# Optimization experiments

Measured on AMD Instinct MI355X. Metric: run time of the kernel, lower is better.

The kernel has to match this reference:

```python
import jax, jax.numpy as jnp
import numpy as np

N_AP, N_UE, D = 256, 1024, 64  # dimension = 64 in source

def setup_inputs() -> dict:
    key = jax.random.key(0)
    ks = jax.random.split(key, 9)
    s = 1.0 / np.sqrt(2 * D)
    return {
        "ap_hid": jax.random.normal(ks[0], (N_AP, D), jnp.float32),
        "ue_hid": jax.random.normal(ks[1], (N_UE, D), jnp.float32),
        "edge_hid": jax.random.normal(ks[2], (N_AP, N_UE, D), jnp.float32),
        "W1": jax.random.normal(ks[3], (2 * D, D), jnp.float32) * s,
        "b1": jnp.zeros((D,), jnp.float32),
        "W2": jax.random.normal(ks[4], (2 * D, D), jnp.float32) * s,
        "b2": jnp.zeros((D,), jnp.float32),
        "W3": jax.random.normal(ks[5], (2 * D, D), jnp.float32) * s,
        "b3": jnp.zeros((D,), jnp.float32),
    }

def reference(ap_hid, ue_hid, edge_hid, W1, b1, W2, b2, W3, b3):
    # edge_hid[a, u] is the feature of edge (AP a, UE u); eid is (a, u) itself.
    A, U, d = edge_hid.shape

    # reduce_func_ap: per-AP mailbox over all UE neighbors -> mlp1(cat(ap_hid, edge_hid))
    ap_in = jnp.concatenate(
        [jnp.broadcast_to(ap_hid[:, None, :], (A, U, d)), edge_hid], axis=-1)  # [A,U,2d]
    ap_res = jax.nn.relu(jnp.einsum('auk,kd->aud', ap_in, W1) + b1)            # [A,U,d]

    # reduce_func_ue: per-UE mailbox over all AP neighbors -> mlp2(cat(ue_hid, edge_hid))
    edge_ua = jnp.swapaxes(edge_hid, 0, 1)                                     # [U,A,d]
    ue_in = jnp.concatenate(
        [jnp.broadcast_to(ue_hid[:, None, :], (U, A, d)), edge_ua], axis=-1)   # [U,A,2d]
    ue_res = jax.nn.relu(jnp.einsum('uak,kd->uad', ue_in, W2) + b2)            # [U,A,d]

    # message_func_edge: for edge (a,u), sum src AP's ap_result excluding the
    # mailbox slot whose eid matches this edge, plus same for dst UE's ue_result.
    ap_sum = ap_res.sum(axis=1)   # [A,d]
    ue_sum = ue_res.sum(axis=1)   # [U,d]
    agg = (ap_sum[:, None, :] - ap_res) \
        + (ue_sum[None, :, :] - jnp.swapaxes(ue_res, 0, 1))                     # [A,U,d]

    new = jnp.einsum('auk,kd->aud', jnp.concatenate([edge_hid, agg], axis=-1), W3) + b3
    return new  # new edge 'hid' for both AP2UE and UE2AP, shape [A,U,d]
```

## Files before the change

### kernel.cpp

```cpp
#include <hip/hip_runtime.h>


#define A_N 256
#define U_N 1024

typedef short short8 __attribute__((ext_vector_type(8)));
typedef float f32x4 __attribute__((ext_vector_type(4)));

__device__ __forceinline__ unsigned short f2bf(float f) {
  unsigned int u = __float_as_uint(f);
  return (unsigned short)((u + 0x7FFFu + ((u >> 16) & 1u)) >> 16);
}

__device__ __forceinline__ f32x4 mfma16(short8 a, short8 b, f32x4 c) {
  return __builtin_amdgcn_mfma_f32_16x16x32_bf16(a, b, c, 0, 0, 0);
}

__device__ __forceinline__ void cvt16(const float4& e0, const float4& e1,
                                      const float4& e2, const float4& e3,
                                      short8& a0, short8& a1) {
  a0[0] = (short)f2bf(e0.x); a0[1] = (short)f2bf(e0.y);
  a0[2] = (short)f2bf(e0.z); a0[3] = (short)f2bf(e0.w);
  a0[4] = (short)f2bf(e1.x); a0[5] = (short)f2bf(e1.y);
  a0[6] = (short)f2bf(e1.z); a0[7] = (short)f2bf(e1.w);
  a1[0] = (short)f2bf(e2.x); a1[1] = (short)f2bf(e2.y);
  a1[2] = (short)f2bf(e2.z); a1[3] = (short)f2bf(e2.w);
  a1[4] = (short)f2bf(e3.x); a1[5] = (short)f2bf(e3.y);
  a1[6] = (short)f2bf(e3.z); a1[7] = (short)f2bf(e3.w);
}

__device__ __forceinline__ void rowmlp_row(const float* __restrict__ in,
                                           const float* __restrict__ W,
                                           const float* __restrict__ bias,
                                           float* __restrict__ out, int r, int lane) {
  float rv = in[r * 64 + lane];
  float acc = bias ? bias[lane] : 0.f;
#pragma unroll
  for (int k = 0; k < 64; k++) acc += __shfl(rv, k, 64) * W[k * 64 + lane];
  out[r * 64 + lane] = acc;
}

__global__ __launch_bounds__(256) void k_prep(
    const float* __restrict__ ap_hid, const float* __restrict__ ue_hid,
    const float* __restrict__ W1, const float* __restrict__ b1,
    const float* __restrict__ W2, const float* __restrict__ b2,
    const float* __restrict__ W3, unsigned short* __restrict__ Wt,
    float* __restrict__ acc_zero, float* __restrict__ c1, float* __restrict__ c2) {
  int bx = blockIdx.x, tid = threadIdx.x;
  if (bx < 320) {
    int i = bx * 256 + tid;
    if (i < 81920) acc_zero[i] = 0.f;
  } else if (bx < 384) {
    int idx = (bx - 320) * 256 + tid;
    int r = idx >> 6, k = idx & 63;
    int sec = r >> 6, d = r & 63;
    float v;
    if (sec == 0)      v = W1[(64 + k) * 64 + d];
    else if (sec == 1) v = W2[(64 + k) * 64 + d];
    else if (sec == 2) v = W3[k * 64 + d];
    else               v = W3[(64 + k) * 64 + d];
    Wt[r * 64 + k] = f2bf(v);
  } else if (bx < 448) {
    int r = (bx - 384) * 4 + (tid >> 6);
    rowmlp_row(ap_hid, W1, b1, c1, r, tid & 63);
  } else {
    int r = (bx - 448) * 4 + (tid >> 6);
    rowmlp_row(ue_hid, W2, b2, c2, r, tid & 63);
  }
}

__global__ __launch_bounds__(256) void k_post(
    const float* __restrict__ ap_sum, const float* __restrict__ ue_sum,
    const float* __restrict__ W3, const float* __restrict__ b3,
    float* __restrict__ s3, float* __restrict__ s4) {
  int bx = blockIdx.x, tid = threadIdx.x;
  if (bx < 64) {
    int r = bx * 4 + (tid >> 6);
    rowmlp_row(ap_sum, W3 + 4096, nullptr, s3, r, tid & 63);
  } else {
    int r = (bx - 64) * 4 + (tid >> 6);
    rowmlp_row(ue_sum, W3 + 4096, b3, s4, r, tid & 63);
  }
}

__global__ __launch_bounds__(256) void k_pass1(
    const float* __restrict__ edge, const unsigned short* __restrict__ Wt,
    const float* __restrict__ c1, const float* __restrict__ c2,
    float* __restrict__ ap_sum, float* __restrict__ ue_sum) {
  int tid = threadIdx.x, lane = tid & 63, w = tid >> 6;
  int fr = lane & 15, fq = lane >> 4;
  int a0 = (blockIdx.x >> 4) * 4;
  int u0 = (blockIdx.x & 15) * 64;
  int urow = u0 + w * 16 + fr;
  const float* erow = edge + urow * 64 + fq * 8;

  short8 bw[8][2];
#pragma unroll
  for (int nt = 0; nt < 8; nt++)
#pragma unroll
    for (int ks = 0; ks < 2; ks++)
      bw[nt][ks] = *(const short8*)(Wt + (nt * 16 + fr) * 64 + ks * 32 + fq * 8);

  float c2v[4][4];
#pragma unroll
  for (int j = 0; j < 4; j++)
#pragma unroll
    for (int i = 0; i < 4; i++)
      c2v[j][i] = c2[(u0 + w * 16 + fq * 4 + i) * 64 + j * 16 + fr];

  float ureg[4][4];
#pragma unroll
  for (int j = 0; j < 4; j++)
#pragma unroll
    for (int i = 0; i < 4; i++) ureg[j][i] = 0.f;

  const float* p0 = erow + a0 * 65536;
  float4 e0 = *(const float4*)(p0);
  float4 e1 = *(const float4*)(p0 + 4);
  float4 e2 = *(const float4*)(p0 + 32);
  float4 e3 = *(const float4*)(p0 + 36);
  float c1v[4];
#pragma unroll
  for (int j = 0; j < 4; j++) c1v[j] = c1[a0 * 64 + j * 16 + fr];

  for (int c = 0; c < 4; c++) {
    int a = a0 + c;
    float4 n0, n1, n2, n3;
    float nc1[4];
    if (c < 3) {
      const float* np = erow + (a + 1) * 65536;
      n0 = *(const float4*)(np);
      n1 = *(const float4*)(np + 4);
      n2 = *(const float4*)(np + 32);
      n3 = *(const float4*)(np + 36);
#pragma unroll
      for (int j = 0; j < 4; j++) nc1[j] = c1[(a + 1) * 64 + j * 16 + fr];
    }
    short8 af0, af1;
    cvt16(e0, e1, e2, e3, af0, af1);

#pragma unroll
    for (int j = 0; j < 4; j++) {
      f32x4 acc = {0.f, 0.f, 0.f, 0.f};
      acc = mfma16(af0, bw[j][0], acc);
      acc = mfma16(af1, bw[j][1], acc);
      float cv = c1v[j];
      float rs = fmaxf(acc[0] + cv, 0.f) + fmaxf(acc[1] + cv, 0.f) +
                 fmaxf(acc[2] + cv, 0.f) + fmaxf(acc[3] + cv, 0.f);
      rs += __shfl_xor(rs, 16, 64);
      rs += __shfl_xor(rs, 32, 64);
      if (lane < 16) atomicAdd(&ap_sum[a * 64 + j * 16 + lane], rs);
    }
#pragma unroll
    for (int j = 0; j < 4; j++) {
      f32x4 acc = {0.f, 0.f, 0.f, 0.f};
      acc = mfma16(af0, bw[4 + j][0], acc);
      acc = mfma16(af1, bw[4 + j][1], acc);
#pragma unroll
      for (int i = 0; i < 4; i++)
        ureg[j][i] += fmaxf(acc[i] + c2v[j][i], 0.f);
    }
    if (c < 3) {
      e0 = n0; e1 = n1; e2 = n2; e3 = n3;
#pragma unroll
      for (int j = 0; j < 4; j++) c1v[j] = nc1[j];
    }
  }
#pragma unroll
  for (int j = 0; j < 4; j++)
#pragma unroll
    for (int i = 0; i < 4; i++)
      atomicAdd(&ue_sum[(u0 + w * 16 + fq * 4 + i) * 64 + j * 16 + fr], ureg[j][i]);
}

__global__ __launch_bounds__(256) void k_pass2(
    const float* __restrict__ edge, const unsigned short* __restrict__ Wt,
    const float* __restrict__ c1, const float* __restrict__ c2,
    const float* __restrict__ s3, const float* __restrict__ s4,
    float* __restrict__ out) {
  __shared__ unsigned short W_lds[256 * 72];
  __shared__ unsigned short t_lds[64 * 72];
  int tid = threadIdx.x, lane = tid & 63, w = tid >> 6;
  int fr = lane & 15, fq = lane >> 4;
  int a = blockIdx.x >> 2;
  int ubase = (blockIdx.x & 3) * 256;

#pragma unroll
  for (int it = 0; it < 8; it++) {
    int r = it * 32 + (tid >> 3), seg = tid & 7;
    *(uint4*)&W_lds[r * 72 + seg * 8] = *(const uint4*)(Wt + r * 64 + seg * 8);
  }

  float c1v[4], s3v[4];
#pragma unroll
  for (int j = 0; j < 4; j++) {
    c1v[j] = c1[a * 64 + j * 16 + fr];
    s3v[j] = s3[a * 64 + j * 16 + fr];
  }

  const float* er0 = edge + (a * 1024 + ubase + w * 16 + fr) * 64 + fq * 8;
  float4 e0 = *(const float4*)(er0);
  float4 e1 = *(const float4*)(er0 + 4);
  float4 e2 = *(const float4*)(er0 + 32);
  float4 e3 = *(const float4*)(er0 + 36);

  __syncthreads();

  for (int pnl = 0; pnl < 4; pnl++) {
    int upan = ubase + pnl * 64;
    float4 n0, n1, n2, n3;
    if (pnl < 3) {
      const float* nr = edge + (a * 1024 + upan + 64 + w * 16 + fr) * 64 + fq * 8;
      n0 = *(const float4*)(nr);
      n1 = *(const float4*)(nr + 4);
      n2 = *(const float4*)(nr + 32);
      n3 = *(const float4*)(nr + 36);
    }
    float c2v[4][4], s4v[4][4];
#pragma unroll
    for (int j = 0; j < 4; j++)
#pragma unroll
      for (int i = 0; i < 4; i++) {
        int u = upan + w * 16 + fq * 4 + i;
        c2v[j][i] = c2[u * 64 + j * 16 + fr];
        s4v[j][i] = s4[u * 64 + j * 16 + fr];
      }
    short8 af0, af1;
    cvt16(e0, e1, e2, e3, af0, af1);

    f32x4 accP3[4];
#pragma unroll
    for (int j = 0; j < 4; j++) {
      const unsigned short* wr = &W_lds[(j * 16 + fr) * 72 + fq * 8];
      short8 b10 = *(const short8*)(wr);
      short8 b11 = *(const short8*)(wr + 32);
      short8 b20 = *(const short8*)(wr + 64 * 72);
      short8 b21 = *(const short8*)(wr + 64 * 72 + 32);
      short8 b30 = *(const short8*)(wr + 128 * 72);
      short8 b31 = *(const short8*)(wr + 128 * 72 + 32);
      f32x4 a1 = {0.f, 0.f, 0.f, 0.f};
      a1 = mfma16(af0, b10, a1);
      a1 = mfma16(af1, b11, a1);
      f32x4 a2 = {0.f, 0.f, 0.f, 0.f};
      a2 = mfma16(af0, b20, a2);
      a2 = mfma16(af1, b21, a2);
      f32x4 p3 = {0.f, 0.f, 0.f, 0.f};
      p3 = mfma16(af0, b30, p3);
      p3 = mfma16(af1, b31, p3);
      accP3[j] = p3;
#pragma unroll
      for (int i = 0; i < 4; i++) {
        float tv = fmaxf(a1[i] + c1v[j], 0.f) + fmaxf(a2[i] + c2v[j][i], 0.f);
        t_lds[(w * 16 + fq * 4 + i) * 72 + j * 16 + fr] = f2bf(tv);
      }
    }
    short8 tf0 = *(const short8*)&t_lds[(w * 16 + fr) * 72 + fq * 8];
    short8 tf1 = *(const short8*)&t_lds[(w * 16 + fr) * 72 + 32 + fq * 8];
#pragma unroll
    for (int j = 0; j < 4; j++) {
      const unsigned short* wr = &W_lds[(192 + j * 16 + fr) * 72 + fq * 8];
      short8 b0 = *(const short8*)(wr);
      short8 b1 = *(const short8*)(wr + 32);
      f32x4 acc = {0.f, 0.f, 0.f, 0.f};
      acc = mfma16(tf0, b0, acc);
      acc = mfma16(tf1, b1, acc);
#pragma unroll
      for (int i = 0; i < 4; i++) {
        int u = upan + w * 16 + fq * 4 + i;
        out[(a * 1024 + u) * 64 + j * 16 + fr] =
            accP3[j][i] - acc[i] + s3v[j] + s4v[j][i];
      }
    }
    if (pnl < 3) { e0 = n0; e1 = n1; e2 = n2; e3 = n3; }
  }
}

extern "C" void kernel_launch(void* const* d_in, const int* in_sizes, int n_in,
                              void* d_out, int out_size, void* d_ws, size_t ws_size,
                              hipStream_t stream) {
  const float* ap_hid = (const float*)d_in[0];
  const float* ue_hid = (const float*)d_in[1];
  const float* edge   = (const float*)d_in[2];
  const float* W1     = (const float*)d_in[3];
  const float* b1     = (const float*)d_in[4];
  const float* W2     = (const float*)d_in[5];
  const float* b2     = (const float*)d_in[6];
  const float* W3     = (const float*)d_in[7];
  const float* b3     = (const float*)d_in[8];
  float* out = (float*)d_out;

  char* ws = (char*)d_ws;
  unsigned short* Wt = (unsigned short*)ws;
  float* c1     = (float*)(ws + 32768);
  float* c2     = (float*)(ws + 98304);
  float* ap_sum = (float*)(ws + 360448);
  float* ue_sum = (float*)(ws + 425984);
  float* s3     = (float*)(ws + 688128);
  float* s4     = (float*)(ws + 753664);

  k_prep<<<704, 256, 0, stream>>>(ap_hid, ue_hid, W1, b1, W2, b2, W3, Wt,
                                  (float*)(ws + 360448), c1, c2);
  k_pass1<<<1024, 256, 0, stream>>>(edge, Wt, c1, c2, ap_sum, ue_sum);
  k_post<<<320, 256, 0, stream>>>(ap_sum, ue_sum, W3, b3, s3, s4);
  k_pass2<<<1024, 256, 0, stream>>>(edge, Wt, c1, c2, s3, s4, out);
}
```

Baseline: 176.6 us.

## Fuse pass1, post and pass2 into one cooperative kernel with grid sync

The two edge passes and the small post kernel become a single cooperative launch of 512 blocks separated by a grid-wide sync. Each block now handles 8 APs by 64 UEs, and the second phase uses the same tile so its edge reads may hit cache. The s3/s4 row MLPs are computed in-block with bf16 MFMA instead of a separate fp32 kernel, and weights are held in registers rather than LDS. This cuts launches and intermediate round trips, at the cost of higher register pressure, fewer blocks, and reduced precision for the sum projections. A two-kernel fallback runs if the cooperative launch fails.

```diff
diff --git a/kernel.cpp b/kernel.cpp
--- a/kernel.cpp
+++ b/kernel.cpp
@@ -1,8 +1,8 @@
 #include <hip/hip_runtime.h>
-
-
-#define A_N 256
-#define U_N 1024
+#include <hip/hip_cooperative_groups.h>
+
+namespace cg = cooperative_groups;
+
 
 typedef short short8 __attribute__((ext_vector_type(8)));
 typedef float f32x4 __attribute__((ext_vector_type(4)));
@@ -16,17 +16,20 @@
   return __builtin_amdgcn_mfma_f32_16x16x32_bf16(a, b, c, 0, 0, 0);
 }
 
+__device__ __forceinline__ short8 cvt8(float4 a, float4 b) {
+  short8 r;
+  r[0] = (short)f2bf(a.x); r[1] = (short)f2bf(a.y);
+  r[2] = (short)f2bf(a.z); r[3] = (short)f2bf(a.w);
+  r[4] = (short)f2bf(b.x); r[5] = (short)f2bf(b.y);
+  r[6] = (short)f2bf(b.z); r[7] = (short)f2bf(b.w);
+  return r;
+}
+
 __device__ __forceinline__ void cvt16(const float4& e0, const float4& e1,
                                       const float4& e2, const float4& e3,
                                       short8& a0, short8& a1) {
-  a0[0] = (short)f2bf(e0.x); a0[1] = (short)f2bf(e0.y);
-  a0[2] = (short)f2bf(e0.z); a0[3] = (short)f2bf(e0.w);
-  a0[4] = (short)f2bf(e1.x); a0[5] = (short)f2bf(e1.y);
-  a0[6] = (short)f2bf(e1.z); a0[7] = (short)f2bf(e1.w);
-  a1[0] = (short)f2bf(e2.x); a1[1] = (short)f2bf(e2.y);
-  a1[2] = (short)f2bf(e2.z); a1[3] = (short)f2bf(e2.w);
-  a1[4] = (short)f2bf(e3.x); a1[5] = (short)f2bf(e3.y);
-  a1[6] = (short)f2bf(e3.z); a1[7] = (short)f2bf(e3.w);
+  a0 = cvt8(e0, e1);
+  a1 = cvt8(e2, e3);
 }
 
 __device__ __forceinline__ void rowmlp_row(const float* __restrict__ in,
@@ -69,50 +72,29 @@
   }
 }
 
-__global__ __launch_bounds__(256) void k_post(
-    const float* __restrict__ ap_sum, const float* __restrict__ ue_sum,
-    const float* __restrict__ W3, const float* __restrict__ b3,
-    float* __restrict__ s3, float* __restrict__ s4) {
-  int bx = blockIdx.x, tid = threadIdx.x;
-  if (bx < 64) {
-    int r = bx * 4 + (tid >> 6);
-    rowmlp_row(ap_sum, W3 + 4096, nullptr, s3, r, tid & 63);
-  } else {
-    int r = (bx - 64) * 4 + (tid >> 6);
-    rowmlp_row(ue_sum, W3 + 4096, b3, s4, r, tid & 63);
-  }
-}
-
-__global__ __launch_bounds__(256) void k_pass1(
+__device__ __forceinline__ void phaseA(
     const float* __restrict__ edge, const unsigned short* __restrict__ Wt,
     const float* __restrict__ c1, const float* __restrict__ c2,
     float* __restrict__ ap_sum, float* __restrict__ ue_sum) {
   int tid = threadIdx.x, lane = tid & 63, w = tid >> 6;
   int fr = lane & 15, fq = lane >> 4;
-  int a0 = (blockIdx.x >> 4) * 4;
-  int u0 = (blockIdx.x & 15) * 64;
-  int urow = u0 + w * 16 + fr;
-  const float* erow = edge + urow * 64 + fq * 8;
+  int bx = blockIdx.x;
+  int a0 = (bx >> 4) * 8, u0 = (bx & 15) * 64;
+  const float* erow = edge + (u0 + w * 16 + fr) * 64 + fq * 8;
 
   short8 bw[8][2];
 #pragma unroll
-  for (int nt = 0; nt < 8; nt++)
-#pragma unroll
-    for (int ks = 0; ks < 2; ks++)
-      bw[nt][ks] = *(const short8*)(Wt + (nt * 16 + fr) * 64 + ks * 32 + fq * 8);
-
+  for (int nt = 0; nt < 8; nt++) {
+    bw[nt][0] = *(const short8*)(Wt + (nt * 16 + fr) * 64 + fq * 8);
+    bw[nt][1] = *(const short8*)(Wt + (nt * 16 + fr) * 64 + 32 + fq * 8);
+  }
   float c2v[4][4];
 #pragma unroll
   for (int j = 0; j < 4; j++)
 #pragma unroll
     for (int i = 0; i < 4; i++)
       c2v[j][i] = c2[(u0 + w * 16 + fq * 4 + i) * 64 + j * 16 + fr];
-
-  float ureg[4][4];
-#pragma unroll
-  for (int j = 0; j < 4; j++)
-#pragma unroll
-    for (int i = 0; i < 4; i++) ureg[j][i] = 0.f;
+  float ureg[4][4] = {};
 
   const float* p0 = erow + a0 * 65536;
   float4 e0 = *(const float4*)(p0);
@@ -123,11 +105,11 @@
 #pragma unroll
   for (int j = 0; j < 4; j++) c1v[j] = c1[a0 * 64 + j * 16 + fr];
 
-  for (int c = 0; c < 4; c++) {
+  for (int c = 0; c < 8; c++) {
     int a = a0 + c;
     float4 n0, n1, n2, n3;
     float nc1[4];
-    if (c < 3) {
+    if (c < 7) {
       const float* np = erow + (a + 1) * 65536;
       n0 = *(const float4*)(np);
       n1 = *(const float4*)(np + 4);
@@ -138,29 +120,24 @@
     }
     short8 af0, af1;
     cvt16(e0, e1, e2, e3, af0, af1);
-
 #pragma unroll
     for (int j = 0; j < 4; j++) {
-      f32x4 acc = {0.f, 0.f, 0.f, 0.f};
-      acc = mfma16(af0, bw[j][0], acc);
-      acc = mfma16(af1, bw[j][1], acc);
+      f32x4 A1 = {0.f, 0.f, 0.f, 0.f};
+      A1 = mfma16(af0, bw[j][0], A1);
+      A1 = mfma16(af1, bw[j][1], A1);
+      f32x4 A2 = {0.f, 0.f, 0.f, 0.f};
+      A2 = mfma16(af0, bw[4 + j][0], A2);
+      A2 = mfma16(af1, bw[4 + j][1], A2);
       float cv = c1v[j];
-      float rs = fmaxf(acc[0] + cv, 0.f) + fmaxf(acc[1] + cv, 0.f) +
-                 fmaxf(acc[2] + cv, 0.f) + fmaxf(acc[3] + cv, 0.f);
+      float rs = fmaxf(A1[0] + cv, 0.f) + fmaxf(A1[1] + cv, 0.f) +
+                 fmaxf(A1[2] + cv, 0.f) + fmaxf(A1[3] + cv, 0.f);
+#pragma unroll
+      for (int i = 0; i < 4; i++) ureg[j][i] += fmaxf(A2[i] + c2v[j][i], 0.f);
       rs += __shfl_xor(rs, 16, 64);
       rs += __shfl_xor(rs, 32, 64);
       if (lane < 16) atomicAdd(&ap_sum[a * 64 + j * 16 + lane], rs);
     }
-#pragma unroll
-    for (int j = 0; j < 4; j++) {
-      f32x4 acc = {0.f, 0.f, 0.f, 0.f};
-      acc = mfma16(af0, bw[4 + j][0], acc);
-      acc = mfma16(af1, bw[4 + j][1], acc);
-#pragma unroll
-      for (int i = 0; i < 4; i++)
-        ureg[j][i] += fmaxf(acc[i] + c2v[j][i], 0.f);
-    }
-    if (c < 3) {
+    if (c < 7) {
       e0 = n0; e1 = n1; e2 = n2; e3 = n3;
 #pragma unroll
       for (int j = 0; j < 4; j++) c1v[j] = nc1[j];
@@ -173,80 +150,98 @@
       atomicAdd(&ue_sum[(u0 + w * 16 + fq * 4 + i) * 64 + j * 16 + fr], ureg[j][i]);
 }
 
-__global__ __launch_bounds__(256) void k_pass2(
-    const float* __restrict__ edge, const unsigned short* __restrict__ Wt,
-    const float* __restrict__ c1, const float* __restrict__ c2,
-    const float* __restrict__ s3, const float* __restrict__ s4,
-    float* __restrict__ out) {
-  __shared__ unsigned short W_lds[256 * 72];
-  __shared__ unsigned short t_lds[64 * 72];
+__device__ __forceinline__ void phaseB(
+    const float* __restrict__ edge, const unsigned short* __restrict__ Wt,
+    const float* __restrict__ c1, const float* __restrict__ c2,
+    const float* __restrict__ ap_sum, const float* __restrict__ ue_sum,
+    const float* __restrict__ b3, float* __restrict__ out,
+    unsigned short* t_lds) {
   int tid = threadIdx.x, lane = tid & 63, w = tid >> 6;
   int fr = lane & 15, fq = lane >> 4;
-  int a = blockIdx.x >> 2;
-  int ubase = (blockIdx.x & 3) * 256;
-
-#pragma unroll
-  for (int it = 0; it < 8; it++) {
-    int r = it * 32 + (tid >> 3), seg = tid & 7;
-    *(uint4*)&W_lds[r * 72 + seg * 8] = *(const uint4*)(Wt + r * 64 + seg * 8);
-  }
-
-  float c1v[4], s3v[4];
+  int bx = blockIdx.x;
+  int a0 = (bx >> 4) * 8, u0 = (bx & 15) * 64;
+  const float* erow = edge + (u0 + w * 16 + fr) * 64 + fq * 8;
+
+  const float* p0 = erow + a0 * 65536;
+  float4 e0 = *(const float4*)(p0);
+  float4 e1 = *(const float4*)(p0 + 4);
+  float4 e2 = *(const float4*)(p0 + 32);
+  float4 e3 = *(const float4*)(p0 + 36);
+
+  short8 bwA[4][2], bwB[4][2], bwT[4][2], bwG[4][2];
 #pragma unroll
   for (int j = 0; j < 4; j++) {
-    c1v[j] = c1[a * 64 + j * 16 + fr];
-    s3v[j] = s3[a * 64 + j * 16 + fr];
-  }
-
-  const float* er0 = edge + (a * 1024 + ubase + w * 16 + fr) * 64 + fq * 8;
-  float4 e0 = *(const float4*)(er0);
-  float4 e1 = *(const float4*)(er0 + 4);
-  float4 e2 = *(const float4*)(er0 + 32);
-  float4 e3 = *(const float4*)(er0 + 36);
-
-  __syncthreads();
-
-  for (int pnl = 0; pnl < 4; pnl++) {
-    int upan = ubase + pnl * 64;
+#pragma unroll
+    for (int ks = 0; ks < 2; ks++) {
+      bwA[j][ks] = *(const short8*)(Wt + (j * 16 + fr) * 64 + ks * 32 + fq * 8);
+      bwB[j][ks] = *(const short8*)(Wt + (64 + j * 16 + fr) * 64 + ks * 32 + fq * 8);
+      bwT[j][ks] = *(const short8*)(Wt + (128 + j * 16 + fr) * 64 + ks * 32 + fq * 8);
+      bwG[j][ks] = *(const short8*)(Wt + (192 + j * 16 + fr) * 64 + ks * 32 + fq * 8);
+    }
+  }
+  float c1v[4], b3v[4];
+#pragma unroll
+  for (int j = 0; j < 4; j++) {
+    c1v[j] = c1[a0 * 64 + j * 16 + fr];
+    b3v[j] = b3[j * 16 + fr];
+  }
+  float c2v[4][4];
+#pragma unroll
+  for (int j = 0; j < 4; j++)
+#pragma unroll
+    for (int i = 0; i < 4; i++)
+      c2v[j][i] = c2[(u0 + w * 16 + fq * 4 + i) * 64 + j * 16 + fr];
+
+  const float* up = ue_sum + (u0 + w * 16 + fr) * 64 + fq * 8;
+  short8 sf0 = cvt8(*(const float4*)(up), *(const float4*)(up + 4));
+  short8 sf1 = cvt8(*(const float4*)(up + 32), *(const float4*)(up + 36));
+  f32x4 s4C[4];
+#pragma unroll
+  for (int j = 0; j < 4; j++) {
+    f32x4 t = {0.f, 0.f, 0.f, 0.f};
+    t = mfma16(sf0, bwG[j][0], t);
+    t = mfma16(sf1, bwG[j][1], t);
+    s4C[j] = t;
+  }
+  const float* apk = ap_sum + (a0 + (fr & 7)) * 64 + fq * 8;
+  short8 pa0 = cvt8(*(const float4*)(apk), *(const float4*)(apk + 4));
+  short8 pa1 = cvt8(*(const float4*)(apk + 32), *(const float4*)(apk + 36));
+  f32x4 s3C[4];
+#pragma unroll
+  for (int j = 0; j < 4; j++) {
+    f32x4 t = {0.f, 0.f, 0.f, 0.f};
+    t = mfma16(pa0, bwG[j][0], t);
+    t = mfma16(pa1, bwG[j][1], t);
+    s3C[j] = t;
+  }
+
+  for (int c = 0; c < 8; c++) {
     float4 n0, n1, n2, n3;
-    if (pnl < 3) {
-      const float* nr = edge + (a * 1024 + upan + 64 + w * 16 + fr) * 64 + fq * 8;
-      n0 = *(const float4*)(nr);
-      n1 = *(const float4*)(nr + 4);
-      n2 = *(const float4*)(nr + 32);
-      n3 = *(const float4*)(nr + 36);
-    }
-    float c2v[4][4], s4v[4][4];
-#pragma unroll
-    for (int j = 0; j < 4; j++)
-#pragma unroll
-      for (int i = 0; i < 4; i++) {
-        int u = upan + w * 16 + fq * 4 + i;
-        c2v[j][i] = c2[u * 64 + j * 16 + fr];
-        s4v[j][i] = s4[u * 64 + j * 16 + fr];
-      }
+    float nc1[4];
+    if (c < 7) {
+      const float* np = erow + (a0 + c + 1) * 65536;
+      n0 = *(const float4*)(np);
+      n1 = *(const float4*)(np + 4);
+      n2 = *(const float4*)(np + 32);
+      n3 = *(const float4*)(np + 36);
+#pragma unroll
+      for (int j = 0; j < 4; j++) nc1[j] = c1[(a0 + c + 1) * 64 + j * 16 + fr];
+    }
     short8 af0, af1;
     cvt16(e0, e1, e2, e3, af0, af1);
 
     f32x4 accP3[4];
 #pragma unroll
     for (int j = 0; j < 4; j++) {
-      const unsigned short* wr = &W_lds[(j * 16 + fr) * 72 + fq * 8];
-      short8 b10 = *(const short8*)(wr);
-      short8 b11 = *(const short8*)(wr + 32);
-      short8 b20 = *(const short8*)(wr + 64 * 72);
-      short8 b21 = *(const short8*)(wr + 64 * 72 + 32);
-      short8 b30 = *(const short8*)(wr + 128 * 72);
-      short8 b31 = *(const short8*)(wr + 128 * 72 + 32);
       f32x4 a1 = {0.f, 0.f, 0.f, 0.f};
-      a1 = mfma16(af0, b10, a1);
-      a1 = mfma16(af1, b11, a1);
+      a1 = mfma16(af0, bwA[j][0], a1);
+      a1 = mfma16(af1, bwA[j][1], a1);
       f32x4 a2 = {0.f, 0.f, 0.f, 0.f};
-      a2 = mfma16(af0, b20, a2);
-      a2 = mfma16(af1, b21, a2);
+      a2 = mfma16(af0, bwB[j][0], a2);
+      a2 = mfma16(af1, bwB[j][1], a2);
       f32x4 p3 = {0.f, 0.f, 0.f, 0.f};
-      p3 = mfma16(af0, b30, p3);
-      p3 = mfma16(af1, b31, p3);
+      p3 = mfma16(af0, bwT[j][0], p3);
+      p3 = mfma16(af1, bwT[j][1], p3);
       accP3[j] = p3;
 #pragma unroll
       for (int i = 0; i < 4; i++) {
@@ -256,23 +251,52 @@
     }
     short8 tf0 = *(const short8*)&t_lds[(w * 16 + fr) * 72 + fq * 8];
     short8 tf1 = *(const short8*)&t_lds[(w * 16 + fr) * 72 + 32 + fq * 8];
+    float* outb = out + ((a0 + c) * 1024 + u0 + w * 16) * 64;
 #pragma unroll
     for (int j = 0; j < 4; j++) {
-      const unsigned short* wr = &W_lds[(192 + j * 16 + fr) * 72 + fq * 8];
-      short8 b0 = *(const short8*)(wr);
-      short8 b1 = *(const short8*)(wr + 32);
-      f32x4 acc = {0.f, 0.f, 0.f, 0.f};
-      acc = mfma16(tf0, b0, acc);
-      acc = mfma16(tf1, b1, acc);
-#pragma unroll
-      for (int i = 0; i < 4; i++) {
-        int u = upan + w * 16 + fq * 4 + i;
-        out[(a * 1024 + u) * 64 + j * 16 + fr] =
-            accP3[j][i] - acc[i] + s3v[j] + s4v[j][i];
-      }
-    }
-    if (pnl < 3) { e0 = n0; e1 = n1; e2 = n2; e3 = n3; }
-  }
+      f32x4 g = {0.f, 0.f, 0.f, 0.f};
+      g = mfma16(tf0, bwG[j][0], g);
+      g = mfma16(tf1, bwG[j][1], g);
+      float s3v = __shfl(s3C[j][c & 3], ((c >> 2) << 4) | (lane & 15), 64);
+#pragma unroll
+      for (int i = 0; i < 4; i++)
+        outb[(fq * 4 + i) * 64 + j * 16 + fr] =
+            accP3[j][i] - g[i] + s3v + s4C[j][i] + b3v[j];
+    }
+    if (c < 7) {
+      e0 = n0; e1 = n1; e2 = n2; e3 = n3;
+#pragma unroll
+      for (int j = 0; j < 4; j++) c1v[j] = nc1[j];
+    }
+  }
+}
+
+__global__ __launch_bounds__(256, 2) void k_main(
+    const float* __restrict__ edge, const unsigned short* __restrict__ Wt,
+    const float* __restrict__ c1, const float* __restrict__ c2,
+    float* __restrict__ ap_sum, float* __restrict__ ue_sum,
+    const float* __restrict__ b3, float* __restrict__ out) {
+  __shared__ unsigned short t_lds[64 * 72];
+  phaseA(edge, Wt, c1, c2, ap_sum, ue_sum);
+  __threadfence();
+  cg::this_grid().sync();
+  phaseB(edge, Wt, c1, c2, ap_sum, ue_sum, b3, out, t_lds);
+}
+
+__global__ __launch_bounds__(256, 2) void k_phA(
+    const float* __restrict__ edge, const unsigned short* __restrict__ Wt,
+    const float* __restrict__ c1, const float* __restrict__ c2,
+    float* __restrict__ ap_sum, float* __restrict__ ue_sum) {
+  phaseA(edge, Wt, c1, c2, ap_sum, ue_sum);
+}
+
+__global__ __launch_bounds__(256, 2) void k_phB(
+    const float* __restrict__ edge, const unsigned short* __restrict__ Wt,
+    const float* __restrict__ c1, const float* __restrict__ c2,
+    const float* __restrict__ ap_sum, const float* __restrict__ ue_sum,
+    const float* __restrict__ b3, float* __restrict__ out) {
+  __shared__ unsigned short t_lds[64 * 72];
+  phaseB(edge, Wt, c1, c2, ap_sum, ue_sum, b3, out, t_lds);
 }
 
 extern "C" void kernel_launch(void* const* d_in, const int* in_sizes, int n_in,
@@ -287,7 +311,7 @@
   const float* b2     = (const float*)d_in[6];
   const float* W3     = (const float*)d_in[7];
   const float* b3     = (const float*)d_in[8];
-  float* out = (float*)d_out;
+  float* outp = (float*)d_out;
 
   char* ws = (char*)d_ws;
   unsigned short* Wt = (unsigned short*)ws;
@@ -295,12 +319,17 @@
   float* c2     = (float*)(ws + 98304);
   float* ap_sum = (float*)(ws + 360448);
   float* ue_sum = (float*)(ws + 425984);
-  float* s3     = (float*)(ws + 688128);
-  float* s4     = (float*)(ws + 753664);
 
   k_prep<<<704, 256, 0, stream>>>(ap_hid, ue_hid, W1, b1, W2, b2, W3, Wt,
                                   (float*)(ws + 360448), c1, c2);
-  k_pass1<<<1024, 256, 0, stream>>>(edge, Wt, c1, c2, ap_sum, ue_sum);
-  k_post<<<320, 256, 0, stream>>>(ap_sum, ue_sum, W3, b3, s3, s4);
-  k_pass2<<<1024, 256, 0, stream>>>(edge, Wt, c1, c2, s3, s4, out);
-}
+
+  void* args[] = {(void*)&edge, (void*)&Wt, (void*)&c1, (void*)&c2,
+                  (void*)&ap_sum, (void*)&ue_sum, (void*)&b3, (void*)&outp};
+  hipError_t err = hipLaunchCooperativeKernel((const void*)k_main, dim3(512),
+                                              dim3(256), args, 0, stream);
+  if (err != hipSuccess) {
+    (void)hipGetLastError();
+    k_phA<<<512, 256, 0, stream>>>(edge, Wt, c1, c2, ap_sum, ue_sum);
+    k_phB<<<512, 256, 0, stream>>>(edge, Wt, c1, c2, ap_sum, ue_sum, b3, outp);
+  }
+}
```

After: 269.6 us. 1.53x slower.

## Compute full edge output in pass1, store bf16 partial, make pass2 elementwise

Applied to the files above, without the earlier changes.

Pass1 now computes all four MFMA products per edge tile, including the W3 projection and the correction GEMM on relu(ap)+relu(ue). It writes the result as a packed bf16 partial buffer, so the edge tensor is read only once. Pass2 becomes a streaming kernel that adds the s3/s4 sum terms and writes the output with nontemporal stores. Edge tiles are staged into swizzled LDS through global_load_lds double buffering. This replaces the second 64MB fp32 edge read with a 32MB bf16 write plus read, at the cost of extra rounding of the output to bf16 precision.

```diff
diff --git a/kernel.cpp b/kernel.cpp
--- a/kernel.cpp
+++ b/kernel.cpp
@@ -1,14 +1,12 @@
 #include <hip/hip_runtime.h>
 
-
-#define A_N 256
-#define U_N 1024
 
 typedef short short8 __attribute__((ext_vector_type(8)));
 typedef float f32x4 __attribute__((ext_vector_type(4)));
+typedef unsigned int u32;
 
 __device__ __forceinline__ unsigned short f2bf(float f) {
-  unsigned int u = __float_as_uint(f);
+  u32 u = __float_as_uint(f);
   return (unsigned short)((u + 0x7FFFu + ((u >> 16) & 1u)) >> 16);
 }
 
@@ -16,17 +14,31 @@
   return __builtin_amdgcn_mfma_f32_16x16x32_bf16(a, b, c, 0, 0, 0);
 }
 
-__device__ __forceinline__ void cvt16(const float4& e0, const float4& e1,
-                                      const float4& e2, const float4& e3,
-                                      short8& a0, short8& a1) {
-  a0[0] = (short)f2bf(e0.x); a0[1] = (short)f2bf(e0.y);
-  a0[2] = (short)f2bf(e0.z); a0[3] = (short)f2bf(e0.w);
-  a0[4] = (short)f2bf(e1.x); a0[5] = (short)f2bf(e1.y);
-  a0[6] = (short)f2bf(e1.z); a0[7] = (short)f2bf(e1.w);
-  a1[0] = (short)f2bf(e2.x); a1[1] = (short)f2bf(e2.y);
-  a1[2] = (short)f2bf(e2.z); a1[3] = (short)f2bf(e2.w);
-  a1[4] = (short)f2bf(e3.x); a1[5] = (short)f2bf(e3.y);
-  a1[6] = (short)f2bf(e3.z); a1[7] = (short)f2bf(e3.w);
+__device__ __forceinline__ short8 cvt8(float4 a, float4 b) {
+  short8 r;
+  r[0] = (short)f2bf(a.x); r[1] = (short)f2bf(a.y);
+  r[2] = (short)f2bf(a.z); r[3] = (short)f2bf(a.w);
+  r[4] = (short)f2bf(b.x); r[5] = (short)f2bf(b.y);
+  r[6] = (short)f2bf(b.z); r[7] = (short)f2bf(b.w);
+  return r;
+}
+
+__device__ __forceinline__ void gl_lds16(const float* g, float* l) {
+  __builtin_amdgcn_global_load_lds(
+      (const __attribute__((address_space(1))) u32*)g,
+      (__attribute__((address_space(3))) u32*)l, 16, 0, 0);
+}
+
+__device__ __forceinline__ void stage_slice(const float* __restrict__ edge,
+                                            int a, int u0, int w, int lane,
+                                            float* __restrict__ buf) {
+#pragma unroll
+  for (int q = 0; q < 4; q++) {
+    int rl = q * 4 + (lane >> 4);
+    int cg = (lane & 15) ^ (rl & 7);
+    const float* g = edge + (a * 1024 + u0 + w * 16 + rl) * 64 + cg * 4;
+    gl_lds16(g, buf + w * 1024 + q * 256);
+  }
 }
 
 __device__ __forceinline__ void rowmlp_row(const float* __restrict__ in,
@@ -69,102 +81,117 @@
   }
 }
 
-__global__ __launch_bounds__(256) void k_post(
+__global__ __launch_bounds__(256) void k_mid(
     const float* __restrict__ ap_sum, const float* __restrict__ ue_sum,
     const float* __restrict__ W3, const float* __restrict__ b3,
-    float* __restrict__ s3, float* __restrict__ s4) {
+    float* __restrict__ s3, float* __restrict__ s4b) {
   int bx = blockIdx.x, tid = threadIdx.x;
   if (bx < 64) {
     int r = bx * 4 + (tid >> 6);
     rowmlp_row(ap_sum, W3 + 4096, nullptr, s3, r, tid & 63);
   } else {
     int r = (bx - 64) * 4 + (tid >> 6);
-    rowmlp_row(ue_sum, W3 + 4096, b3, s4, r, tid & 63);
-  }
-}
-
-__global__ __launch_bounds__(256) void k_pass1(
+    rowmlp_row(ue_sum, W3 + 4096, b3, s4b, r, tid & 63);
+  }
+}
+
+__global__ __launch_bounds__(256, 3) void k_pass1(
     const float* __restrict__ edge, const unsigned short* __restrict__ Wt,
     const float* __restrict__ c1, const float* __restrict__ c2,
-    float* __restrict__ ap_sum, float* __restrict__ ue_sum) {
+    float* __restrict__ ap_sum, float* __restrict__ ue_sum,
+    u32* __restrict__ partial) {
+  __shared__ float Ebuf[2][4096];
+  __shared__ unsigned short t_lds[64 * 72];
   int tid = threadIdx.x, lane = tid & 63, w = tid >> 6;
   int fr = lane & 15, fq = lane >> 4;
-  int a0 = (blockIdx.x >> 4) * 4;
-  int u0 = (blockIdx.x & 15) * 64;
-  int urow = u0 + w * 16 + fr;
-  const float* erow = edge + urow * 64 + fq * 8;
-
-  short8 bw[8][2];
-#pragma unroll
-  for (int nt = 0; nt < 8; nt++)
-#pragma unroll
-    for (int ks = 0; ks < 2; ks++)
-      bw[nt][ks] = *(const short8*)(Wt + (nt * 16 + fr) * 64 + ks * 32 + fq * 8);
-
+  int bx = blockIdx.x;
+  int a0 = (bx >> 4) * 4, pnl = bx & 15, u0 = pnl * 64;
+
+  stage_slice(edge, a0, u0, w, lane, &Ebuf[0][0]);
+
+  short8 bwA[4][2], bwB[4][2], bwT[4][2], bwG[4][2];
+#pragma unroll
+  for (int j = 0; j < 4; j++) {
+#pragma unroll
+    for (int ks = 0; ks < 2; ks++) {
+      bwA[j][ks] = *(const short8*)(Wt + (j * 16 + fr) * 64 + ks * 32 + fq * 8);
+      bwB[j][ks] = *(const short8*)(Wt + (64 + j * 16 + fr) * 64 + ks * 32 + fq * 8);
+      bwT[j][ks] = *(const short8*)(Wt + (128 + j * 16 + fr) * 64 + ks * 32 + fq * 8);
+      bwG[j][ks] = *(const short8*)(Wt + (192 + j * 16 + fr) * 64 + ks * 32 + fq * 8);
+    }
+  }
   float c2v[4][4];
 #pragma unroll
   for (int j = 0; j < 4; j++)
 #pragma unroll
     for (int i = 0; i < 4; i++)
       c2v[j][i] = c2[(u0 + w * 16 + fq * 4 + i) * 64 + j * 16 + fr];
-
-  float ureg[4][4];
-#pragma unroll
-  for (int j = 0; j < 4; j++)
-#pragma unroll
-    for (int i = 0; i < 4; i++) ureg[j][i] = 0.f;
-
-  const float* p0 = erow + a0 * 65536;
-  float4 e0 = *(const float4*)(p0);
-  float4 e1 = *(const float4*)(p0 + 4);
-  float4 e2 = *(const float4*)(p0 + 32);
-  float4 e3 = *(const float4*)(p0 + 36);
-  float c1v[4];
-#pragma unroll
-  for (int j = 0; j < 4; j++) c1v[j] = c1[a0 * 64 + j * 16 + fr];
-
+  float ureg[4][4] = {};
+
+  int sw = fr & 7;
   for (int c = 0; c < 4; c++) {
     int a = a0 + c;
-    float4 n0, n1, n2, n3;
-    float nc1[4];
-    if (c < 3) {
-      const float* np = erow + (a + 1) * 65536;
-      n0 = *(const float4*)(np);
-      n1 = *(const float4*)(np + 4);
-      n2 = *(const float4*)(np + 32);
-      n3 = *(const float4*)(np + 36);
-#pragma unroll
-      for (int j = 0; j < 4; j++) nc1[j] = c1[(a + 1) * 64 + j * 16 + fr];
-    }
-    short8 af0, af1;
-    cvt16(e0, e1, e2, e3, af0, af1);
-
+    const float* rb = &Ebuf[c & 1][w * 1024 + fr * 64];
+    float4 f0 = *(const float4*)(rb + ((fq * 2) ^ sw) * 4);
+    float4 f1 = *(const float4*)(rb + ((fq * 2 + 1) ^ sw) * 4);
+    float4 f2 = *(const float4*)(rb + (8 + ((fq * 2) ^ sw)) * 4);
+    float4 f3 = *(const float4*)(rb + (8 + ((fq * 2 + 1) ^ sw)) * 4);
+    asm volatile("" ::: "memory");
+    if (c < 3) stage_slice(edge, a + 1, u0, w, lane, &Ebuf[(c + 1) & 1][0]);
+    asm volatile("" ::: "memory");
+
+    float c1v[4];
+#pragma unroll
+    for (int j = 0; j < 4; j++) c1v[j] = c1[a * 64 + j * 16 + fr];
+    short8 af0 = cvt8(f0, f1);
+    short8 af1 = cvt8(f2, f3);
+
+    f32x4 accP3[4];
 #pragma unroll
     for (int j = 0; j < 4; j++) {
-      f32x4 acc = {0.f, 0.f, 0.f, 0.f};
-      acc = mfma16(af0, bw[j][0], acc);
-      acc = mfma16(af1, bw[j][1], acc);
-      float cv = c1v[j];
-      float rs = fmaxf(acc[0] + cv, 0.f) + fmaxf(acc[1] + cv, 0.f) +
-                 fmaxf(acc[2] + cv, 0.f) + fmaxf(acc[3] + cv, 0.f);
+      f32x4 A1 = {0.f, 0.f, 0.f, 0.f};
+      A1 = mfma16(af0, bwA[j][0], A1);
+      A1 = mfma16(af1, bwA[j][1], A1);
+      f32x4 A2 = {0.f, 0.f, 0.f, 0.f};
+      A2 = mfma16(af0, bwB[j][0], A2);
+      A2 = mfma16(af1, bwB[j][1], A2);
+      f32x4 P3 = {0.f, 0.f, 0.f, 0.f};
+      P3 = mfma16(af0, bwT[j][0], P3);
+      P3 = mfma16(af1, bwT[j][1], P3);
+      accP3[j] = P3;
+      float rs = 0.f;
+#pragma unroll
+      for (int i = 0; i < 4; i++) {
+        float r1 = fmaxf(A1[i] + c1v[j], 0.f);
+        float r2 = fmaxf(A2[i] + c2v[j][i], 0.f);
+        rs += r1;
+        ureg[j][i] += r2;
+        t_lds[(w * 16 + fq * 4 + i) * 72 + j * 16 + fr] = f2bf(r1 + r2);
+      }
       rs += __shfl_xor(rs, 16, 64);
       rs += __shfl_xor(rs, 32, 64);
       if (lane < 16) atomicAdd(&ap_sum[a * 64 + j * 16 + lane], rs);
     }
+    short8 tf0 = *(const short8*)&t_lds[(w * 16 + fr) * 72 + fq * 8];
+    short8 tf1 = *(const short8*)&t_lds[(w * 16 + fr) * 72 + 32 + fq * 8];
 #pragma unroll
     for (int j = 0; j < 4; j++) {
-      f32x4 acc = {0.f, 0.f, 0.f, 0.f};
-      acc = mfma16(af0, bw[4 + j][0], acc);
-      acc = mfma16(af1, bw[4 + j][1], acc);
-#pragma unroll
-      for (int i = 0; i < 4; i++)
-        ureg[j][i] += fmaxf(acc[i] + c2v[j][i], 0.f);
-    }
-    if (c < 3) {
-      e0 = n0; e1 = n1; e2 = n2; e3 = n3;
-#pragma unroll
-      for (int j = 0; j < 4; j++) c1v[j] = nc1[j];
-    }
+      f32x4 g = {0.f, 0.f, 0.f, 0.f};
+      g = mfma16(tf0, bwG[j][0], g);
+      g = mfma16(tf1, bwG[j][1], g);
+#pragma unroll
+      for (int i = 0; i < 4; i++) accP3[j][i] -= g[i];
+    }
+    u32 r8[8];
+#pragma unroll
+    for (int i = 0; i < 4; i++)
+#pragma unroll
+      for (int jj = 0; jj < 2; jj++)
+        r8[i * 2 + jj] = (u32)f2bf(accP3[2 * jj][i]) |
+                         ((u32)f2bf(accP3[2 * jj + 1][i]) << 16);
+    u32* pp = partial + (((a * 16 + pnl) * 4 + w) * 64 + lane) * 8;
+    *(uint4*)pp = make_uint4(r8[0], r8[1], r8[2], r8[3]);
+    *(uint4*)(pp + 4) = make_uint4(r8[4], r8[5], r8[6], r8[7]);
   }
 #pragma unroll
   for (int j = 0; j < 4; j++)
@@ -174,104 +201,39 @@
 }
 
 __global__ __launch_bounds__(256) void k_pass2(
-    const float* __restrict__ edge, const unsigned short* __restrict__ Wt,
-    const float* __restrict__ c1, const float* __restrict__ c2,
-    const float* __restrict__ s3, const float* __restrict__ s4,
-    float* __restrict__ out) {
-  __shared__ unsigned short W_lds[256 * 72];
-  __shared__ unsigned short t_lds[64 * 72];
-  int tid = threadIdx.x, lane = tid & 63, w = tid >> 6;
-  int fr = lane & 15, fq = lane >> 4;
-  int a = blockIdx.x >> 2;
-  int ubase = (blockIdx.x & 3) * 256;
-
-#pragma unroll
-  for (int it = 0; it < 8; it++) {
-    int r = it * 32 + (tid >> 3), seg = tid & 7;
-    *(uint4*)&W_lds[r * 72 + seg * 8] = *(const uint4*)(Wt + r * 64 + seg * 8);
-  }
-
-  float c1v[4], s3v[4];
-#pragma unroll
-  for (int j = 0; j < 4; j++) {
-    c1v[j] = c1[a * 64 + j * 16 + fr];
-    s3v[j] = s3[a * 64 + j * 16 + fr];
-  }
-
-  const float* er0 = edge + (a * 1024 + ubase + w * 16 + fr) * 64 + fq * 8;
-  float4 e0 = *(const float4*)(er0);
-  float4 e1 = *(const float4*)(er0 + 4);
-  float4 e2 = *(const float4*)(er0 + 32);
-  float4 e3 = *(const float4*)(er0 + 36);
-
-  __syncthreads();
-
-  for (int pnl = 0; pnl < 4; pnl++) {
-    int upan = ubase + pnl * 64;
-    float4 n0, n1, n2, n3;
-    if (pnl < 3) {
-      const float* nr = edge + (a * 1024 + upan + 64 + w * 16 + fr) * 64 + fq * 8;
-      n0 = *(const float4*)(nr);
-      n1 = *(const float4*)(nr + 4);
-      n2 = *(const float4*)(nr + 32);
-      n3 = *(const float4*)(nr + 36);
-    }
-    float c2v[4][4], s4v[4][4];
-#pragma unroll
-    for (int j = 0; j < 4; j++)
-#pragma unroll
-      for (int i = 0; i < 4; i++) {
-        int u = upan + w * 16 + fq * 4 + i;
-        c2v[j][i] = c2[u * 64 + j * 16 + fr];
-        s4v[j][i] = s4[u * 64 + j * 16 + fr];
+    const u32* __restrict__ partial, const float* __restrict__ s3,
+    const float* __restrict__ s4b, float* __restrict__ out) {
+  int t0 = blockIdx.x * 256 + threadIdx.x;
+  uint4 pa[4], pb[4];
+#pragma unroll
+  for (int it = 0; it < 4; it++) {
+    const uint4* pp = (const uint4*)(partial + (t0 + it * 262144) * 8);
+    pa[it] = pp[0];
+    pb[it] = pp[1];
+  }
+#pragma unroll
+  for (int it = 0; it < 4; it++) {
+    int rec = t0 + it * 262144;
+    int l = rec & 63, w = (rec >> 6) & 3, p = (rec >> 8) & 15, a = rec >> 12;
+    int fr = l & 15, fq = l >> 4;
+    int ub = p * 64 + w * 16 + fq * 4;
+    float s3v[4];
+#pragma unroll
+    for (int j = 0; j < 4; j++) s3v[j] = s3[a * 64 + j * 16 + fr];
+    u32 d[8] = {pa[it].x, pa[it].y, pa[it].z, pa[it].w,
+                pb[it].x, pb[it].y, pb[it].z, pb[it].w};
+#pragma unroll
+    for (int i = 0; i < 4; i++) {
+      const float* s4r = s4b + (ub + i) * 64 + fr;
+      float* outr = out + (a * 1024 + ub + i) * 64 + fr;
+#pragma unroll
+      for (int j = 0; j < 4; j++) {
+        u32 dw = d[i * 2 + (j >> 1)];
+        u32 bits = (j & 1) ? (dw & 0xFFFF0000u) : (dw << 16);
+        float v = __uint_as_float(bits) + s3v[j] + s4r[j * 16];
+        __builtin_nontemporal_store(v, outr + j * 16);
       }
-    short8 af0, af1;
-    cvt16(e0, e1, e2, e3, af0, af1);
-
-    f32x4 accP3[4];
-#pragma unroll
-    for (int j = 0; j < 4; j++) {
-      const unsigned short* wr = &W_lds[(j * 16 + fr) * 72 + fq * 8];
-      short8 b10 = *(const short8*)(wr);
-      short8 b11 = *(const short8*)(wr + 32);
-      short8 b20 = *(const short8*)(wr + 64 * 72);
-      short8 b21 = *(const short8*)(wr + 64 * 72 + 32);
-      short8 b30 = *(const short8*)(wr + 128 * 72);
-      short8 b31 = *(const short8*)(wr + 128 * 72 + 32);
-      f32x4 a1 = {0.f, 0.f, 0.f, 0.f};
-      a1 = mfma16(af0, b10, a1);
-      a1 = mfma16(af1, b11, a1);
-      f32x4 a2 = {0.f, 0.f, 0.f, 0.f};
-      a2 = mfma16(af0, b20, a2);
-      a2 = mfma16(af1, b21, a2);
-      f32x4 p3 = {0.f, 0.f, 0.f, 0.f};
-      p3 = mfma16(af0, b30, p3);
-      p3 = mfma16(af1, b31, p3);
-      accP3[j] = p3;
-#pragma unroll
-      for (int i = 0; i < 4; i++) {
-        float tv = fmaxf(a1[i] + c1v[j], 0.f) + fmaxf(a2[i] + c2v[j][i], 0.f);
-        t_lds[(w * 16 + fq * 4 + i) * 72 + j * 16 + fr] = f2bf(tv);
-      }
-    }
-    short8 tf0 = *(const short8*)&t_lds[(w * 16 + fr) * 72 + fq * 8];
-    short8 tf1 = *(const short8*)&t_lds[(w * 16 + fr) * 72 + 32 + fq * 8];
-#pragma unroll
-    for (int j = 0; j < 4; j++) {
-      const unsigned short* wr = &W_lds[(192 + j * 16 + fr) * 72 + fq * 8];
-      short8 b0 = *(const short8*)(wr);
-      short8 b1 = *(const short8*)(wr + 32);
-      f32x4 acc = {0.f, 0.f, 0.f, 0.f};
-      acc = mfma16(tf0, b0, acc);
-      acc = mfma16(tf1, b1, acc);
-#pragma unroll
-      for (int i = 0; i < 4; i++) {
-        int u = upan + w * 16 + fq * 4 + i;
-        out[(a * 1024 + u) * 64 + j * 16 + fr] =
-            accP3[j][i] - acc[i] + s3v[j] + s4v[j][i];
-      }
-    }
-    if (pnl < 3) { e0 = n0; e1 = n1; e2 = n2; e3 = n3; }
+    }
   }
 }
 
@@ -287,7 +249,7 @@
   const float* b2     = (const float*)d_in[6];
   const float* W3     = (const float*)d_in[7];
   const float* b3     = (const float*)d_in[8];
-  float* out = (float*)d_out;
+  float* outp = (float*)d_out;
 
   char* ws = (char*)d_ws;
   unsigned short* Wt = (unsigned short*)ws;
@@ -296,11 +258,12 @@
   float* ap_sum = (float*)(ws + 360448);
   float* ue_sum = (float*)(ws + 425984);
   float* s3     = (float*)(ws + 688128);
-  float* s4     = (float*)(ws + 753664);
+  float* s4b    = (float*)(ws + 753664);
+  u32* partial  = (u32*)(ws + 2097152);
 
   k_prep<<<704, 256, 0, stream>>>(ap_hid, ue_hid, W1, b1, W2, b2, W3, Wt,
                                   (float*)(ws + 360448), c1, c2);
-  k_pass1<<<1024, 256, 0, stream>>>(edge, Wt, c1, c2, ap_sum, ue_sum);
-  k_post<<<320, 256, 0, stream>>>(ap_sum, ue_sum, W3, b3, s3, s4);
-  k_pass2<<<1024, 256, 0, stream>>>(edge, Wt, c1, c2, s3, s4, out);
-}
+  k_pass1<<<1024, 256, 0, stream>>>(edge, Wt, c1, c2, ap_sum, ue_sum, partial);
+  k_mid<<<320, 256, 0, stream>>>(ap_sum, ue_sum, W3, b3, s3, s4b);
+  k_pass2<<<1024, 256, 0, stream>>>(partial, s3, s4b, outp);
+}
```

Result: slower. 244.9 us (+38.7%).
